# Kernel optimization log

Measured on AMD Instinct MI355X. Metric: run time of the kernel, lower is better.

## Reference

```python
import jax, jax.numpy as jnp
import numpy as np

K_SIZE = 3            # kernel_size
PAD = K_SIZE // 2     # zero padding on each side
EPS = 1e-5            # torch layer_norm default eps


def setup_inputs() -> dict:
    key = jax.random.key(0)
    ks = jax.random.split(key, 9)
    B, C, H, W = 4, 256, 64, 64
    Cout = 256
    sc = 1.0 / np.sqrt(C)
    return {
        "x":  jax.random.normal(ks[0], (B, C, H, W), dtype=jnp.float32),
        "Wq": jax.random.normal(ks[1], (C, C), dtype=jnp.float32) * sc,
        "bq": jax.random.normal(ks[2], (C,), dtype=jnp.float32) * 0.02,
        "Wk": jax.random.normal(ks[3], (C, C), dtype=jnp.float32) * sc,
        "bk": jax.random.normal(ks[4], (C,), dtype=jnp.float32) * 0.02,
        "Wv": jax.random.normal(ks[5], (C, C), dtype=jnp.float32) * sc,
        "bv": jax.random.normal(ks[6], (C,), dtype=jnp.float32) * 0.02,
        "Wo": jax.random.normal(ks[7], (C, Cout), dtype=jnp.float32) * sc,
        "bo": jax.random.normal(ks[8], (Cout,), dtype=jnp.float32) * 0.02,
    }


def _forward(x, Wq, bq, Wk, bk, Wv, bv, Wo, bo):
    B, C, H, W = x.shape
    # F.layer_norm(x, [H, W]): normalize over last two dims per (b, c), no affine
    mean = jnp.mean(x, axis=(2, 3), keepdims=True)
    var = jnp.var(x, axis=(2, 3), keepdims=True)
    xn = (x - mean) * jax.lax.rsqrt(var + EPS)
    # zero pad spatial dims
    p = jnp.pad(xn, ((0, 0), (0, 0), (PAD, PAD), (PAD, PAD)))
    # channels-last for per-pixel linears
    p = jnp.transpose(p, (0, 2, 3, 1))          # [B, Hp, Wp, C]
    xc = jnp.transpose(xn, (0, 2, 3, 1))        # [B, H,  W,  C] (window centers)
    scale = jnp.asarray(C, x.dtype) ** -0.5     # depth_scale = C**-0.5
    q = (xc @ Wq + bq) * scale                  # [B, H, W, C] (center-token query)
    kf = p @ Wk + bk                            # [B, Hp, Wp, C]
    vf = p @ Wv + bv
    # gather the kk=9 shifted views -> window tokens per pixel
    Kw = jnp.stack([kf[:, dh:dh + H, dw:dw + W, :]
                    for dh in range(K_SIZE) for dw in range(K_SIZE)], axis=3)  # [B,H,W,kk,C]
    Vw = jnp.stack([vf[:, dh:dh + H, dw:dw + W, :]
                    for dh in range(K_SIZE) for dw in range(K_SIZE)], axis=3)
    logits = jnp.einsum('bhwc,bhwnc->bhwn', q, Kw)     # [B, H, W, kk]
    attn = jax.nn.softmax(logits, axis=-1)
    ctx = jnp.einsum('bhwn,bhwnc->bhwc', attn, Vw)     # [B, H, W, C]
    out = ctx @ Wo + bo                                # [B, H, W, Cout]
    return jnp.transpose(out, (0, 3, 1, 2))            # [B, Cout, H, W]


def reference(x, Wq, bq, Wk, bk, Wv, bv, Wo, bo):
    return _forward(x, Wq, bq, Wk, bk, Wv, bv, Wo, bo)
```

## Files before the change

kernel.cpp:

```cpp
#include <hip/hip_runtime.h>
#include <hip/hip_bf16.h>
#include <stdint.h>

typedef __bf16 bf16x8 __attribute__((ext_vector_type(8)));
typedef float f32x4 __attribute__((ext_vector_type(4)));

#define KDIM 256
#define NPIX 16384
#define QKVS 768

__device__ __forceinline__ float b2f(ushort u){
    union { float f; uint32_t i; } x; x.i = ((uint32_t)u) << 16; return x.f;
}
__device__ __forceinline__ ushort f2b(float f){
    uint32_t u = __float_as_uint(f);
    uint32_t r = (u + 0x7fffu + ((u >> 16) & 1u)) >> 16;
    return (ushort)r;
}
__device__ __forceinline__ void unpack2(uint d, float& lo, float& hi){
    lo = __uint_as_float(d << 16);
    hi = __uint_as_float(d & 0xffff0000u);
}
__device__ __forceinline__ uint cvtpk(float lo, float hi){
    uint r;
    asm volatile("v_cvt_pk_bf16_f32 %0, %1, %2" : "=v"(r) : "v"(lo), "v"(hi));
    return r;
}

__global__ __launch_bounds__(256)
void ln_fuse(const float* __restrict__ x, ushort* __restrict__ xt,
             float* __restrict__ psum, float* __restrict__ psum2){
    __shared__ ushort sh[128 * 68];
    __shared__ float ssum[16 * 132], ssum2[16 * 132];
    const int bid = blockIdx.x;
    const int b = bid >> 7, rem = bid & 127, h = rem >> 1, ch = (rem & 1) * 128;
    const int tid = threadIdx.x;
    const int csub = tid >> 4, w4 = tid & 15;
#pragma unroll
    for (int i = 0; i < 8; ++i){
        int c = csub + 16 * i;
        float4 v = *(const float4*)(x + ((size_t)(b * 256 + ch + c)) * 4096
                                      + h * 64 + w4 * 4);
        ushort4 u; u.x = f2b(v.x); u.y = f2b(v.y); u.z = f2b(v.z); u.w = f2b(v.w);
        *(ushort4*)&sh[c * 68 + w4 * 4] = u;
        ssum [w4 * 132 + c] = v.x + v.y + v.z + v.w;
        ssum2[w4 * 132 + c] = v.x * v.x + v.y * v.y + v.z * v.z + v.w * v.w;
    }
    __syncthreads();
    if (tid < 128){
        float S = 0.f, S2 = 0.f;
#pragma unroll
        for (int j = 0; j < 16; ++j){ S += ssum[j * 132 + tid]; S2 += ssum2[j * 132 + tid]; }
        psum [(b * 64 + h) * 256 + ch + tid] = S;
        psum2[(b * 64 + h) * 256 + ch + tid] = S2;
    }
    const int c16 = tid & 15, w16 = tid >> 4;
#pragma unroll
    for (int p = 0; p < 4; ++p){
        int w = p * 16 + w16;
        union { ushort u[8]; uint4 v; } r;
#pragma unroll
        for (int j = 0; j < 8; ++j) r.u[j] = sh[(c16 * 8 + j) * 68 + w];
        size_t row = (size_t)(b * 4096 + h * 64 + w);
        *(uint4*)(xt + row * 256 + ch + c16 * 8) = r.v;
    }
}

__global__ __launch_bounds__(256)
void prep2(const float* __restrict__ Wq, const float* __restrict__ bq,
           const float* __restrict__ Wk, const float* __restrict__ bk,
           const float* __restrict__ Wv, const float* __restrict__ bv,
           const float* __restrict__ Wo,
           const float* __restrict__ psum, const float* __restrict__ psum2,
           ushort* __restrict__ wtq, ushort* __restrict__ wot,
           float* __restrict__ biasp, ushort* __restrict__ qkv){
    __shared__ float shW[32 * 33];
    __shared__ float shS[8 * 32], shS2[8 * 32], shRV[4 * 32], shM[256];
    const int bid = blockIdx.x, tid = threadIdx.x;
    if (bid < 192){
        int mat = bid / 64, tile = bid % 64;
        int ti = tile & 7, tj = tile >> 3;
        {
            int kk = tid & 31, idx = tid >> 5;
            int b = idx >> 1, h0 = (idx & 1) * 32;
            float S = 0.f, S2 = 0.f;
            for (int r = 0; r < 32; ++r){
                int off = (b * 64 + h0 + r) * 256 + tj * 32 + kk;
                S += psum[off]; S2 += psum2[off];
            }
            shS[idx * 32 + kk] = S; shS2[idx * 32 + kk] = S2;
        }
        __syncthreads();
        if (tid < 128){
            int b = tid >> 5, kk = tid & 31;
            float S  = shS [(b * 2) * 32 + kk] + shS [(b * 2 + 1) * 32 + kk];
            float S2 = shS2[(b * 2) * 32 + kk] + shS2[(b * 2 + 1) * 32 + kk];
            float m = S * (1.f / 4096.f);
            float v = S2 * (1.f / 4096.f) - m * m;
            shRV[b * 32 + kk] = rsqrtf(v + 1e-5f);
        }
        const float* src = (mat == 0) ? Wq : (mat == 1) ? Wk : Wv;
        float qs = (mat == 0) ? 0.0625f : 1.0f;
        int tx = tid & 31, ty = tid >> 5;
#pragma unroll
        for (int i = 0; i < 4; ++i)
            shW[(ty + i * 8) * 33 + tx] =
                src[(size_t)(tj * 32 + ty + i * 8) * 256 + ti * 32 + tx] * qs;
        __syncthreads();
#pragma unroll
        for (int b = 0; b < 4; ++b){
            float rv = shRV[b * 32 + tx];
#pragma unroll
            for (int i = 0; i < 4; ++i){
                int n = mat * 256 + ti * 32 + ty + i * 8;
                wtq[((size_t)b * 768 + n) * 256 + tj * 32 + tx] =
                    f2b(shW[tx * 33 + ty + i * 8] * rv);
            }
        }
    } else if (bid < 256){
        int tile = bid - 192;
        int ti = tile & 7, tj = tile >> 3;
        int tx = tid & 31, ty = tid >> 5;
#pragma unroll
        for (int i = 0; i < 4; ++i)
            shW[(ty + i * 8) * 33 + tx] =
                Wo[(size_t)(tj * 32 + ty + i * 8) * 256 + ti * 32 + tx];
        __syncthreads();
#pragma unroll
        for (int i = 0; i < 4; ++i)
            wot[(size_t)(ti * 32 + ty + i * 8) * 256 + tj * 32 + tx] =
                f2b(shW[tx * 33 + ty + i * 8]);
    } else if (bid < 268){
        int t = bid - 256;
        int b = t / 3, mat = t % 3;
        float S = 0.f, S2 = 0.f;
        for (int h = 0; h < 64; ++h){
            S += psum[(b * 64 + h) * 256 + tid]; S2 += psum2[(b * 64 + h) * 256 + tid];
        }
        float m = S * (1.f / 4096.f);
        float v = S2 * (1.f / 4096.f) - m * m;
        shM[tid] = m * rsqrtf(v + 1e-5f);
        __syncthreads();
        const float* W  = (mat == 0) ? Wq : (mat == 1) ? Wk : Wv;
        const float* bb = (mat == 0) ? bq : (mat == 1) ? bk : bv;
        float qs = (mat == 0) ? 0.0625f : 1.0f;
        float acc = 0.f;
        for (int c = 0; c < 256; ++c)
            acc += shM[c] * W[(size_t)c * 256 + tid];
        biasp[b * 768 + mat * 256 + tid] = (bb[tid] - acc) * qs;
    } else {
        ushort* pad = qkv + (size_t)NPIX * QKVS;
        pad[tid]       = 0;
        pad[256 + tid] = f2b(bk[tid]);
        pad[512 + tid] = f2b(bv[tid]);
    }
}

__global__ __launch_bounds__(512, 1)
void gemm_qkv(const ushort* __restrict__ X, const ushort* __restrict__ Y,
              const float* __restrict__ bias, ushort* __restrict__ zb){
    __shared__ ushort ldsA[2][256 * 64];
    __shared__ ushort ldsB[2][256 * 64];
    const int tid  = threadIdx.x;
    const int lane = tid & 63;
    const int wid  = tid >> 6;
    const int wm   = wid >> 2;
    const int wn   = wid & 3;
    const int id    = blockIdx.x;
    const int mtile = id & 63, ntile = id >> 6;
    const int x0 = mtile * 256, y0 = ntile * 256;
    const int bsel = x0 >> 12;
    const ushort* Yb   = Y + ((size_t)bsel * QKVS + y0) * 256;
    const float* biasb = bias + bsel * QKVS;

    auto stage = [&](int buf, int k0){
#pragma unroll
        for (int i = 0; i < 4; ++i){
            int f   = i * 512 + tid;
            int row = f >> 3, cp = f & 7;
            int cs  = cp ^ (row & 7);
            const ushort* ga = X  + (size_t)(x0 + row) * KDIM + k0 + cs * 8;
            const ushort* gb = Yb + (size_t)row        * KDIM + k0 + cs * 8;
            __builtin_amdgcn_global_load_lds(
                (const __attribute__((address_space(1))) void*)ga,
                (__attribute__((address_space(3))) void*)&ldsA[buf][f * 8], 16, 0, 0);
            __builtin_amdgcn_global_load_lds(
                (const __attribute__((address_space(1))) void*)gb,
                (__attribute__((address_space(3))) void*)&ldsB[buf][f * 8], 16, 0, 0);
        }
    };

    f32x4 acc[8][4];
#pragma unroll
    for (int i = 0; i < 8; ++i)
#pragma unroll
        for (int j = 0; j < 4; ++j) acc[i][j] = f32x4{0.f, 0.f, 0.f, 0.f};

    stage(0, 0);
    stage(1, 64);
#pragma unroll
    for (int t = 0; t < 4; ++t){
        if (t < 3) asm volatile("s_waitcnt vmcnt(8)" ::: "memory");
        else       asm volatile("s_waitcnt vmcnt(0)" ::: "memory");
        __builtin_amdgcn_sched_barrier(0);
        __builtin_amdgcn_s_barrier();
        __builtin_amdgcn_sched_barrier(0);
        const int buf = t & 1;
        __builtin_amdgcn_s_setprio(1);
#pragma unroll
        for (int kk = 0; kk < 2; ++kk){
            bf16x8 af[8], bf[4];
#pragma unroll
            for (int fm = 0; fm < 8; ++fm){
                int r = wm * 128 + fm * 16 + (lane & 15);
                int c = kk * 4 + (lane >> 4);
                af[fm] = *(const bf16x8*)&ldsA[buf][(r * 8 + (c ^ (r & 7))) * 8];
            }
#pragma unroll
            for (int fn = 0; fn < 4; ++fn){
                int r = wn * 64 + fn * 16 + (lane & 15);
                int c = kk * 4 + (lane >> 4);
                bf[fn] = *(const bf16x8*)&ldsB[buf][(r * 8 + (c ^ (r & 7))) * 8];
            }
#pragma unroll
            for (int fm = 0; fm < 8; ++fm)
#pragma unroll
                for (int fn = 0; fn < 4; ++fn)
                    acc[fm][fn] = __builtin_amdgcn_mfma_f32_16x16x32_bf16(
                        af[fm], bf[fn], acc[fm][fn], 0, 0, 0);
        }
        __builtin_amdgcn_s_setprio(0);
        __builtin_amdgcn_sched_barrier(0);
        __builtin_amdgcn_s_barrier();
        __builtin_amdgcn_sched_barrier(0);
        if (t < 2) stage(t & 1, (t + 2) * 64);
    }

#pragma unroll
    for (int fm = 0; fm < 8; ++fm){
#pragma unroll
        for (int fn = 0; fn < 4; ++fn){
            int xr = x0 + wm * 128 + fm * 16 + ((lane >> 4) << 2);
            int yc = y0 + wn * 64 + fn * 16 + (lane & 15);
            float bv = biasb[yc];
#pragma unroll
            for (int r = 0; r < 4; ++r)
                zb[(size_t)(xr + r) * QKVS + yc] = f2b(acc[fm][fn][r] + bv);
        }
    }
}

__global__ __launch_bounds__(256)
void attn_win(const ushort* __restrict__ qkv, ushort* __restrict__ ctx){
    const int tid = threadIdx.x;
    const int lane = tid & 63, wid = tid >> 6;
    const int l16 = lane & 15, pg = lane >> 4;
    const int pix = blockIdx.x * 16 + wid * 4 + pg;
    const int b = pix >> 12, hw = pix & 4095;
    const int h = hw >> 6, w = hw & 63;
    const uint PADOFF = (uint)NPIX * QKVS;
    const int cbase = l16 * 16;

    const ushort* qp = qkv + (size_t)pix * QKVS + cbase;
    uint4 qa = *(const uint4*)qp;
    uint4 qb = *(const uint4*)(qp + 8);
    float qf[16];
    unpack2(qa.x, qf[0], qf[1]);  unpack2(qa.y, qf[2], qf[3]);
    unpack2(qa.z, qf[4], qf[5]);  unpack2(qa.w, qf[6], qf[7]);
    unpack2(qb.x, qf[8], qf[9]);  unpack2(qb.y, qf[10], qf[11]);
    unpack2(qb.z, qf[12], qf[13]); unpack2(qb.w, qf[14], qf[15]);

    float lg[9];
    uint roff[9];
#pragma unroll
    for (int n = 0; n < 9; ++n){
        int nh = h + n / 3 - 1, nw = w + n % 3 - 1;
        bool ok = ((unsigned)nh < 64u) & ((unsigned)nw < 64u);
        roff[n] = ok ? (uint)(((b << 12) + (nh << 6) + nw) * QKVS) : PADOFF;
        const ushort* kp = qkv + roff[n] + 256 + cbase;
        uint4 ka = *(const uint4*)kp;
        uint4 kb = *(const uint4*)(kp + 8);
        float kf[16];
        unpack2(ka.x, kf[0], kf[1]);  unpack2(ka.y, kf[2], kf[3]);
        unpack2(ka.z, kf[4], kf[5]);  unpack2(ka.w, kf[6], kf[7]);
        unpack2(kb.x, kf[8], kf[9]);  unpack2(kb.y, kf[10], kf[11]);
        unpack2(kb.z, kf[12], kf[13]); unpack2(kb.w, kf[14], kf[15]);
        float d = 0.f;
#pragma unroll
        for (int j = 0; j < 16; ++j) d += qf[j] * kf[j];
        d += __shfl_xor(d, 1); d += __shfl_xor(d, 2);
        d += __shfl_xor(d, 4); d += __shfl_xor(d, 8);
        lg[n] = d;
    }
    float m = lg[0];
#pragma unroll
    for (int n = 1; n < 9; ++n) m = fmaxf(m, lg[n]);
    float e[9], s = 0.f;
#pragma unroll
    for (int n = 0; n < 9; ++n){ e[n] = __expf(lg[n] - m); s += e[n]; }
    float inv = 1.f / s;

    float c[16];
#pragma unroll
    for (int j = 0; j < 16; ++j) c[j] = 0.f;
#pragma unroll
    for (int n = 0; n < 9; ++n){
        float a = e[n] * inv;
        const ushort* vp = qkv + roff[n] + 512 + cbase;
        uint4 va = *(const uint4*)vp;
        uint4 vb = *(const uint4*)(vp + 8);
        float vf[16];
        unpack2(va.x, vf[0], vf[1]);  unpack2(va.y, vf[2], vf[3]);
        unpack2(va.z, vf[4], vf[5]);  unpack2(va.w, vf[6], vf[7]);
        unpack2(vb.x, vf[8], vf[9]);  unpack2(vb.y, vf[10], vf[11]);
        unpack2(vb.z, vf[12], vf[13]); unpack2(vb.w, vf[14], vf[15]);
#pragma unroll
        for (int j = 0; j < 16; ++j) c[j] += a * vf[j];
    }
    uint4 oa, ob;
    oa.x = cvtpk(c[0], c[1]);   oa.y = cvtpk(c[2], c[3]);
    oa.z = cvtpk(c[4], c[5]);   oa.w = cvtpk(c[6], c[7]);
    ob.x = cvtpk(c[8], c[9]);   ob.y = cvtpk(c[10], c[11]);
    ob.z = cvtpk(c[12], c[13]); ob.w = cvtpk(c[14], c[15]);
    ushort* op = ctx + (size_t)pix * 256 + cbase;
    *(uint4*)op = oa;
    *(uint4*)(op + 8) = ob;
}

__global__ __launch_bounds__(256, 2)
void gemm_out(const ushort* __restrict__ X, const ushort* __restrict__ Y,
              const float* __restrict__ bias, float* __restrict__ zf){
    __shared__ ushort ldsX[2][128 * 64];
    __shared__ ushort ldsY[2][128 * 64];
    const int tid  = threadIdx.x;
    const int lane = tid & 63;
    const int wid  = tid >> 6;
    const int wm   = wid >> 1, wn = wid & 1;
    const int x0   = blockIdx.x * 128, y0 = blockIdx.y * 128;

    auto stage = [&](int buf, int k0){
#pragma unroll
        for (int i = 0; i < 4; ++i){
            int f   = i * 256 + tid;
            int row = f >> 3, cp = f & 7;
            int cs  = cp ^ (row & 7);
            const ushort* gx = X + (size_t)(x0 + row) * KDIM + k0 + cs * 8;
            const ushort* gy = Y + (size_t)(y0 + row) * KDIM + k0 + cs * 8;
            __builtin_amdgcn_global_load_lds(
                (const __attribute__((address_space(1))) void*)gx,
                (__attribute__((address_space(3))) void*)&ldsX[buf][f * 8], 16, 0, 0);
            __builtin_amdgcn_global_load_lds(
                (const __attribute__((address_space(1))) void*)gy,
                (__attribute__((address_space(3))) void*)&ldsY[buf][f * 8], 16, 0, 0);
        }
    };

    f32x4 acc[4][4];
#pragma unroll
    for (int i = 0; i < 4; ++i)
#pragma unroll
        for (int j = 0; j < 4; ++j) acc[i][j] = f32x4{0.f, 0.f, 0.f, 0.f};

    stage(0, 0);
    int buf = 0;
    for (int t = 0; t < 4; ++t){
        __syncthreads();
        if (t < 3) stage(buf ^ 1, (t + 1) * 64);
#pragma unroll
        for (int kk = 0; kk < 2; ++kk){
            bf16x8 xa[4], yb[4];
#pragma unroll
            for (int fm = 0; fm < 4; ++fm){
                int r = wm * 64 + fm * 16 + (lane & 15);
                int c = kk * 4 + (lane >> 4);
                xa[fm] = *(const bf16x8*)&ldsX[buf][(r * 8 + (c ^ (r & 7))) * 8];
            }
#pragma unroll
            for (int fn = 0; fn < 4; ++fn){
                int r = wn * 64 + fn * 16 + (lane & 15);
                int c = kk * 4 + (lane >> 4);
                yb[fn] = *(const bf16x8*)&ldsY[buf][(r * 8 + (c ^ (r & 7))) * 8];
            }
#pragma unroll
            for (int fm = 0; fm < 4; ++fm)
#pragma unroll
                for (int fn = 0; fn < 4; ++fn)
                    acc[fm][fn] = __builtin_amdgcn_mfma_f32_16x16x32_bf16(
                        xa[fm], yb[fn], acc[fm][fn], 0, 0, 0);
        }
        buf ^= 1;
    }

#pragma unroll
    for (int fm = 0; fm < 4; ++fm){
#pragma unroll
        for (int fn = 0; fn < 4; ++fn){
            int xr = x0 + wm * 64 + fm * 16 + ((lane >> 4) << 2);
            int yc = y0 + wn * 64 + fn * 16 + (lane & 15);
            int bpix = yc >> 12, hw = yc & 4095;
#pragma unroll
            for (int r = 0; r < 4; ++r){
                int ch = xr + r;
                zf[((size_t)(bpix * 256 + ch)) * 4096 + hw] =
                    acc[fm][fn][r] + bias[ch];
            }
        }
    }
}

extern "C" void kernel_launch(void* const* d_in, const int* in_sizes, int n_in,
                              void* d_out, int out_size, void* d_ws, size_t ws_size,
                              hipStream_t stream){
    const float* x  = (const float*)d_in[0];
    const float* Wq = (const float*)d_in[1];
    const float* bq = (const float*)d_in[2];
    const float* Wk = (const float*)d_in[3];
    const float* bk = (const float*)d_in[4];
    const float* Wv = (const float*)d_in[5];
    const float* bv = (const float*)d_in[6];
    const float* Wo = (const float*)d_in[7];
    const float* bo = (const float*)d_in[8];
    float* out = (float*)d_out;

    char* ws = (char*)d_ws;
    ushort* wtq    = (ushort*)(ws);
    ushort* wot    = (ushort*)(ws + 1572864);
    float*  biasp  = (float*) (ws + 1703936);
    float*  psum   = (float*) (ws + 1716224);
    float*  psum2  = (float*) (ws + 1978368);
    ushort* xt     = (ushort*)(ws + 2240512);
    ushort* qkv    = (ushort*)(ws + 10629120);
    ushort* ctx    = (ushort*)(ws + 35796480);

    ln_fuse<<<512, 256, 0, stream>>>(x, xt, psum, psum2);
    prep2<<<269, 256, 0, stream>>>(Wq, bq, Wk, bk, Wv, bv, Wo,
                                   psum, psum2, wtq, wot, biasp, qkv);

    gemm_qkv<<<192, 512, 0, stream>>>(xt, wtq, biasp, qkv);

    attn_win<<<1024, 256, 0, stream>>>(qkv, ctx);

    dim3 g2(2, 128);
    gemm_out<<<g2, 256, 0, stream>>>(wot, ctx, bo, out);
}
```

Baseline: 58.04 us.

## Fuse windowed attention with output projection via LDS-resident context tile

Merges the window-attention kernel and the output GEMM into one kernel. Each block computes context for 32 pixels, stores it swizzled in shared memory, then runs MFMA against Wo read directly from global memory and writes the NCHW output. This removes the ctx round trip through global memory and one launch. In exchange, every block re-reads the full 256x256 bf16 Wo from global/L2 without LDS staging, and the GEMM tiles are small.

```diff
diff --git a/kernel.cpp b/kernel.cpp
--- a/kernel.cpp
+++ b/kernel.cpp
@@ -250,12 +250,15 @@
     }
 }
 
-__global__ __launch_bounds__(256)
-void attn_win(const ushort* __restrict__ qkv, ushort* __restrict__ ctx){
+__global__ __launch_bounds__(512, 4)
+void attn_out2(const ushort* __restrict__ qkv, const ushort* __restrict__ wot,
+               const float* __restrict__ bo, float* __restrict__ out){
+    __shared__ ushort ctx[32 * 256];
     const int tid = threadIdx.x;
     const int lane = tid & 63, wid = tid >> 6;
     const int l16 = lane & 15, pg = lane >> 4;
-    const int pix = blockIdx.x * 16 + wid * 4 + pg;
+    const int p = wid * 4 + pg;
+    const int pix = blockIdx.x * 32 + p;
     const int b = pix >> 12, hw = pix & 4095;
     const int h = hw >> 6, w = hw & 63;
     const uint PADOFF = (uint)NPIX * QKVS;
@@ -322,87 +325,48 @@
     oa.z = cvtpk(c[4], c[5]);   oa.w = cvtpk(c[6], c[7]);
     ob.x = cvtpk(c[8], c[9]);   ob.y = cvtpk(c[10], c[11]);
     ob.z = cvtpk(c[12], c[13]); ob.w = cvtpk(c[14], c[15]);
-    ushort* op = ctx + (size_t)pix * 256 + cbase;
-    *(uint4*)op = oa;
-    *(uint4*)(op + 8) = ob;
-}
-
-__global__ __launch_bounds__(256, 2)
-void gemm_out(const ushort* __restrict__ X, const ushort* __restrict__ Y,
-              const float* __restrict__ bias, float* __restrict__ zf){
-    __shared__ ushort ldsX[2][128 * 64];
-    __shared__ ushort ldsY[2][128 * 64];
-    const int tid  = threadIdx.x;
-    const int lane = tid & 63;
-    const int wid  = tid >> 6;
-    const int wm   = wid >> 1, wn = wid & 1;
-    const int x0   = blockIdx.x * 128, y0 = blockIdx.y * 128;
-
-    auto stage = [&](int buf, int k0){
-#pragma unroll
-        for (int i = 0; i < 4; ++i){
-            int f   = i * 256 + tid;
-            int row = f >> 3, cp = f & 7;
-            int cs  = cp ^ (row & 7);
-            const ushort* gx = X + (size_t)(x0 + row) * KDIM + k0 + cs * 8;
-            const ushort* gy = Y + (size_t)(y0 + row) * KDIM + k0 + cs * 8;
-            __builtin_amdgcn_global_load_lds(
-                (const __attribute__((address_space(1))) void*)gx,
-                (__attribute__((address_space(3))) void*)&ldsX[buf][f * 8], 16, 0, 0);
-            __builtin_amdgcn_global_load_lds(
-                (const __attribute__((address_space(1))) void*)gy,
-                (__attribute__((address_space(3))) void*)&ldsY[buf][f * 8], 16, 0, 0);
-        }
-    };
-
-    f32x4 acc[4][4];
-#pragma unroll
-    for (int i = 0; i < 4; ++i)
-#pragma unroll
-        for (int j = 0; j < 4; ++j) acc[i][j] = f32x4{0.f, 0.f, 0.f, 0.f};
-
-    stage(0, 0);
-    int buf = 0;
-    for (int t = 0; t < 4; ++t){
-        __syncthreads();
-        if (t < 3) stage(buf ^ 1, (t + 1) * 64);
-#pragma unroll
-        for (int kk = 0; kk < 2; ++kk){
-            bf16x8 xa[4], yb[4];
-#pragma unroll
-            for (int fm = 0; fm < 4; ++fm){
-                int r = wm * 64 + fm * 16 + (lane & 15);
-                int c = kk * 4 + (lane >> 4);
-                xa[fm] = *(const bf16x8*)&ldsX[buf][(r * 8 + (c ^ (r & 7))) * 8];
-            }
-#pragma unroll
-            for (int fn = 0; fn < 4; ++fn){
-                int r = wn * 64 + fn * 16 + (lane & 15);
-                int c = kk * 4 + (lane >> 4);
-                yb[fn] = *(const bf16x8*)&ldsY[buf][(r * 8 + (c ^ (r & 7))) * 8];
-            }
-#pragma unroll
-            for (int fm = 0; fm < 4; ++fm)
-#pragma unroll
-                for (int fn = 0; fn < 4; ++fn)
-                    acc[fm][fn] = __builtin_amdgcn_mfma_f32_16x16x32_bf16(
-                        xa[fm], yb[fn], acc[fm][fn], 0, 0, 0);
-        }
-        buf ^= 1;
-    }
-
-#pragma unroll
-    for (int fm = 0; fm < 4; ++fm){
-#pragma unroll
-        for (int fn = 0; fn < 4; ++fn){
-            int xr = x0 + wm * 64 + fm * 16 + ((lane >> 4) << 2);
-            int yc = y0 + wn * 64 + fn * 16 + (lane & 15);
-            int bpix = yc >> 12, hw = yc & 4095;
+    *(uint4*)&ctx[p * 256 + (((l16 * 2)     ^ (p & 7)) * 8)] = oa;
+    *(uint4*)&ctx[p * 256 + (((l16 * 2 + 1) ^ (p & 7)) * 8)] = ob;
+    __syncthreads();
+
+    f32x4 acc2[2][2];
+    acc2[0][0] = f32x4{0,0,0,0}; acc2[0][1] = f32x4{0,0,0,0};
+    acc2[1][0] = f32x4{0,0,0,0}; acc2[1][1] = f32x4{0,0,0,0};
+#pragma unroll
+    for (int kk = 0; kk < 8; ++kk){
+        const int ck = kk * 4 + (lane >> 4);
+        bf16x8 af[2], bf[2];
+#pragma unroll
+        for (int fm = 0; fm < 2; ++fm){
+            int r = wid * 32 + fm * 16 + (lane & 15);
+            af[fm] = *(const bf16x8*)(wot + (size_t)r * 256 + ck * 8);
+        }
+#pragma unroll
+        for (int fn = 0; fn < 2; ++fn){
+            int pr = fn * 16 + (lane & 15);
+            bf[fn] = *(const bf16x8*)&ctx[pr * 256 + ((ck ^ (pr & 7)) * 8)];
+        }
+#pragma unroll
+        for (int fm = 0; fm < 2; ++fm)
+#pragma unroll
+            for (int fn = 0; fn < 2; ++fn)
+                acc2[fm][fn] = __builtin_amdgcn_mfma_f32_16x16x32_bf16(
+                    af[fm], bf[fn], acc2[fm][fn], 0, 0, 0);
+    }
+
+    const int bblk = (blockIdx.x * 32) >> 12;
+    const int hwb  = (blockIdx.x * 32) & 4095;
+#pragma unroll
+    for (int fm = 0; fm < 2; ++fm){
+#pragma unroll
+        for (int fn = 0; fn < 2; ++fn){
+            int ch0   = wid * 32 + fm * 16 + ((lane >> 4) << 2);
+            int wpix  = fn * 16 + (lane & 15);
 #pragma unroll
             for (int r = 0; r < 4; ++r){
-                int ch = xr + r;
-                zf[((size_t)(bpix * 256 + ch)) * 4096 + hw] =
-                    acc[fm][fn][r] + bias[ch];
+                int ch = ch0 + r;
+                out[((size_t)(bblk * 256 + ch)) * 4096 + hwb + wpix] =
+                    acc2[fm][fn][r] + bo[ch];
             }
         }
     }
@@ -430,7 +394,6 @@
     float*  psum2  = (float*) (ws + 1978368);
     ushort* xt     = (ushort*)(ws + 2240512);
     ushort* qkv    = (ushort*)(ws + 10629120);
-    ushort* ctx    = (ushort*)(ws + 35796480);
 
     ln_fuse<<<512, 256, 0, stream>>>(x, xt, psum, psum2);
     prep2<<<269, 256, 0, stream>>>(Wq, bq, Wk, bk, Wv, bv, Wo,
@@ -438,8 +401,5 @@
 
     gemm_qkv<<<192, 512, 0, stream>>>(xt, wtq, biasp, qkv);
 
-    attn_win<<<1024, 256, 0, stream>>>(qkv, ctx);
-
-    dim3 g2(2, 128);
-    gemm_out<<<g2, 256, 0, stream>>>(wot, ctx, bo, out);
-}
+    attn_out2<<<512, 512, 0, stream>>>(qkv, wot, bo, out);
+}
```

New measurement: 59.04 us. No clear change (+1.7%).

## Stage QKV GEMM epilogue through LDS and remap block tiles for XCD locality

Applied to the files above, without the earlier changes.

The QKV GEMM epilogue now writes the bias-added bf16 results into a padded shared-memory tile, then stores each output row with coalesced 16-byte writes, replacing scattered 2-byte global stores. Shared memory is merged into one padded array so the same space serves both the double buffers and the output staging. Block indices in both GEMMs are remapped so that blocks landing on the same XCD (every eighth block) work on neighbouring tiles, which should improve L2 reuse of the shared operands. The padded array is larger than the old buffers, and the epilogue adds an extra barrier and a round trip through LDS.

```diff
diff --git a/kernel.cpp b/kernel.cpp
--- a/kernel.cpp
+++ b/kernel.cpp
@@ -159,15 +159,14 @@
 __global__ __launch_bounds__(512, 1)
 void gemm_qkv(const ushort* __restrict__ X, const ushort* __restrict__ Y,
               const float* __restrict__ bias, ushort* __restrict__ zb){
-    __shared__ ushort ldsA[2][256 * 64];
-    __shared__ ushort ldsB[2][256 * 64];
+    __shared__ ushort lds[256 * 264];
     const int tid  = threadIdx.x;
     const int lane = tid & 63;
     const int wid  = tid >> 6;
     const int wm   = wid >> 2;
     const int wn   = wid & 3;
-    const int id    = blockIdx.x;
-    const int mtile = id & 63, ntile = id >> 6;
+    const int tile  = (blockIdx.x & 7) * 24 + (blockIdx.x >> 3);
+    const int mtile = tile / 3, ntile = tile % 3;
     const int x0 = mtile * 256, y0 = ntile * 256;
     const int bsel = x0 >> 12;
     const ushort* Yb   = Y + ((size_t)bsel * QKVS + y0) * 256;
@@ -183,10 +182,12 @@
             const ushort* gb = Yb + (size_t)row        * KDIM + k0 + cs * 8;
             __builtin_amdgcn_global_load_lds(
                 (const __attribute__((address_space(1))) void*)ga,
-                (__attribute__((address_space(3))) void*)&ldsA[buf][f * 8], 16, 0, 0);
+                (__attribute__((address_space(3))) void*)&lds[buf * 16384 + f * 8],
+                16, 0, 0);
             __builtin_amdgcn_global_load_lds(
                 (const __attribute__((address_space(1))) void*)gb,
-                (__attribute__((address_space(3))) void*)&ldsB[buf][f * 8], 16, 0, 0);
+                (__attribute__((address_space(3))) void*)&lds[32768 + buf * 16384 + f * 8],
+                16, 0, 0);
         }
     };
 
@@ -214,13 +215,13 @@
             for (int fm = 0; fm < 8; ++fm){
                 int r = wm * 128 + fm * 16 + (lane & 15);
                 int c = kk * 4 + (lane >> 4);
-                af[fm] = *(const bf16x8*)&ldsA[buf][(r * 8 + (c ^ (r & 7))) * 8];
+                af[fm] = *(const bf16x8*)&lds[buf * 16384 + (r * 8 + (c ^ (r & 7))) * 8];
             }
 #pragma unroll
             for (int fn = 0; fn < 4; ++fn){
                 int r = wn * 64 + fn * 16 + (lane & 15);
                 int c = kk * 4 + (lane >> 4);
-                bf[fn] = *(const bf16x8*)&ldsB[buf][(r * 8 + (c ^ (r & 7))) * 8];
+                bf[fn] = *(const bf16x8*)&lds[32768 + buf * 16384 + (r * 8 + (c ^ (r & 7))) * 8];
             }
 #pragma unroll
             for (int fm = 0; fm < 8; ++fm)
@@ -238,15 +239,24 @@
 
 #pragma unroll
     for (int fm = 0; fm < 8; ++fm){
+        const int r_loc = wm * 128 + fm * 16 + ((lane >> 4) << 2);
 #pragma unroll
         for (int fn = 0; fn < 4; ++fn){
-            int xr = x0 + wm * 128 + fm * 16 + ((lane >> 4) << 2);
-            int yc = y0 + wn * 64 + fn * 16 + (lane & 15);
-            float bv = biasb[yc];
+            const int c_loc = wn * 64 + fn * 16 + (lane & 15);
+            const float bv = biasb[y0 + c_loc];
 #pragma unroll
             for (int r = 0; r < 4; ++r)
-                zb[(size_t)(xr + r) * QKVS + yc] = f2b(acc[fm][fn][r] + bv);
-        }
+                lds[(r_loc + r) * 264 + c_loc] = f2b(acc[fm][fn][r] + bv);
+        }
+    }
+    __syncthreads();
+    {
+        const int row = tid >> 1, half = tid & 1;
+        const ushort* src = &lds[row * 264 + half * 128];
+        ushort* dst = zb + (size_t)(x0 + row) * QKVS + y0 + half * 128;
+#pragma unroll
+        for (int i = 0; i < 16; ++i)
+            *(uint4*)(dst + i * 8) = *(const uint4*)(src + i * 8);
     }
 }
 
@@ -336,7 +346,9 @@
     const int lane = tid & 63;
     const int wid  = tid >> 6;
     const int wm   = wid >> 1, wn = wid & 1;
-    const int x0   = blockIdx.x * 128, y0 = blockIdx.y * 128;
+    const int tile = (blockIdx.x & 7) * 32 + (blockIdx.x >> 3);
+    const int x0   = (tile & 1) * 128;
+    const int y0   = (tile >> 1) * 128;
 
     auto stage = [&](int buf, int k0){
 #pragma unroll
@@ -440,6 +452,5 @@
 
     attn_win<<<1024, 256, 0, stream>>>(qkv, ctx);
 
-    dim3 g2(2, 128);
-    gemm_out<<<g2, 256, 0, stream>>>(wot, ctx, bo, out);
-}
+    gemm_out<<<256, 256, 0, stream>>>(wot, ctx, bo, out);
+}
```

Result: slower. 63.69 us (+9.7%).
